# Performance work log

Measured on AMD Instinct MI355X. Metric: run time of the kernel, lower is better.

## Reference

```python
import jax, jax.numpy as jnp
import numpy as np

N_ENT = 30000
ALL_REL = 221
N_DIM = 32
L = 2
EVAL_REL = 86
B = 16
E = 120000


def setup_inputs() -> dict:
    key = jax.random.key(0)
    ks = jax.random.split(key, 16)
    d = N_DIM
    inp = {
        'head': jax.random.randint(ks[0], (B,), 0, N_ENT),
        'tail': jax.random.randint(ks[1], (B,), 0, N_ENT),
        'edge_heads': jax.random.randint(ks[2], (E,), 0, N_ENT),
        'edge_tails': jax.random.randint(ks[3], (E,), 0, N_ENT),
        'edge_rels': jax.random.randint(ks[4], (E,), 0, ALL_REL),
        'edge_weight': jnp.ones((E,), jnp.float32),
        # learned params (xavier-ish scale)
        'ent_emb': jax.random.normal(ks[5], (N_ENT, d), jnp.float32) * 0.05,
        'rel_embs': jax.random.normal(ks[6], (L, ALL_REL, d), jnp.float32) * 0.1,
        'Wlin': jax.random.normal(ks[7], (L, d, d), jnp.float32) * (1.0 / np.sqrt(d)),
        'blin': jnp.zeros((L, d), jnp.float32),
        'Wrel': jax.random.normal(ks[8], (L, 2 * d, 5), jnp.float32) * 0.1,
        'brel': jnp.zeros((L, 5), jnp.float32),
        'Watt': jax.random.normal(ks[9], (L, 5, ALL_REL), jnp.float32) * 0.3,
        'batt': jnp.zeros((L, ALL_REL), jnp.float32),
        'Wr': jax.random.normal(ks[10], (4 * d, EVAL_REL), jnp.float32) * 0.1,
        'br': jnp.zeros((EVAL_REL,), jnp.float32),
    }
    return inp


def _propagate(init_emb, init_idx, ht_embed, rel_embs, Wlin, blin, Wrel, brel,
               Watt, batt, edge_weight, eh, et, er):
    # init_emb: (B, d); hiddens: (n_ent, B, d)
    Bn, d = init_emb.shape
    hid = jnp.zeros((N_ENT, Bn, d), init_emb.dtype)
    hid = hid.at[init_idx, jnp.arange(Bn)].set(init_emb)
    for l in range(L):
        # per-sample relation attention weights: (B, all_rel)
        relw = jax.nn.sigmoid(jax.nn.relu(ht_embed @ Wrel[l] + brel[l]) @ Watt[l] + batt[l])
        # generalized rspmm: out[t] += w * (relw[:, r] * rel_emb[r]) * hid[h]
        msg = hid[eh] * (relw.T[er][:, :, None] * rel_embs[l][er][:, None, :])  # (E, B, d)
        msg = msg * edge_weight[:, None, None]
        hid = jax.ops.segment_sum(msg, et, num_segments=N_ENT)  # (n_ent, B, d)
        hid = jax.nn.relu(hid @ Wlin[l] + blin[l])
    return hid


def reference(head, tail, edge_heads, edge_tails, edge_rels, edge_weight,
              ent_emb, rel_embs, Wlin, blin, Wrel, brel, Watt, batt, Wr, br):
    head_embed = ent_emb[head]  # (B, d)
    tail_embed = ent_emb[tail]
    ht_embed = jnp.concatenate([head_embed, tail_embed], axis=-1)  # (B, 2d)

    # head -> tail propagation
    hid = _propagate(head_embed, head, ht_embed, rel_embs, Wlin, blin, Wrel, brel,
                     Watt, batt, edge_weight, edge_heads, edge_tails, edge_rels)
    tail_hid = hid[tail, jnp.arange(tail.shape[0])]  # (B, d)

    # tail -> head propagation (same KG, same layers, per original code)
    hid = _propagate(tail_embed, tail, ht_embed, rel_embs, Wlin, blin, Wrel, brel,
                     Watt, batt, edge_weight, edge_heads, edge_tails, edge_rels)
    head_hid = hid[head, jnp.arange(head.shape[0])]

    embeddings = jnp.concatenate([head_embed, tail_embed, head_hid, tail_hid], axis=1)
    return embeddings @ Wr + br  # (B, eval_rel)
```

## Files before the change

kernel.cpp:

```cpp
#include <hip/hip_runtime.h>
#include <math.h>

#define N_ENTC 30000
#define ALL_RELC 221
#define NDIM 32
#define EVAL_RELC 86
#define BB 16
#define NE 120000
#define ROW 512
#define NSCAN 120
#define EPB 1000
#define MW 938


__global__ __launch_bounds__(512) void k_scan(
    const int* __restrict__ head, const int* __restrict__ tail,
    const int* __restrict__ eh, const int* __restrict__ et,
    const int* __restrict__ er, const float* __restrict__ ew,
    const float* __restrict__ ent_emb,
    const float* __restrict__ Wrel, const float* __restrict__ brel,
    const float* __restrict__ Watt, const float* __restrict__ batt,
    int4* __restrict__ recs, int* __restrict__ counts,
    float* __restrict__ relwG, float* __restrict__ hidB,
    float* __restrict__ qaccB, unsigned* __restrict__ ticket)
{
    __shared__ unsigned mH[MW], mT[MW];
    __shared__ int s_src[32];
    __shared__ int s_cnt[4];
    __shared__ float s_ht[BB * 64];
    __shared__ float s_h5[BB * 5];
    const int t = threadIdx.x, bid = blockIdx.x;

    if (t < 32) s_src[t] = (t < BB) ? head[t] : tail[t - BB];
    for (int i = t; i < MW; i += 512) { mH[i] = 0u; mT[i] = 0u; }
    if (t < 4) s_cnt[t] = 0;
    __syncthreads();
    if (t < BB) {
        int h = s_src[t], q = s_src[BB + t];
        atomicOr(&mH[h >> 5], 1u << (h & 31));
        atomicOr(&mT[q >> 5], 1u << (q & 31));
    }
    __syncthreads();

    const int e0 = bid * EPB;
    const int4* eh4 = (const int4*)(eh + e0);
    const int4* et4 = (const int4*)(et + e0);
    for (int p = t; p < EPB / 4; p += 512) {
        int4 h4 = eh4[p], t4 = et4[p];
        int hv[4] = {h4.x, h4.y, h4.z, h4.w};
        int tv[4] = {t4.x, t4.y, t4.z, t4.w};
#pragma unroll
        for (int c = 0; c < 4; c++) {
            int e = e0 + 4 * p + c, h = hv[c], tt = tv[c];
            bool hH = (mH[h >> 5] >> (h & 31)) & 1u;
            bool hT = (mT[h >> 5] >> (h & 31)) & 1u;
            bool tT = (mT[tt >> 5] >> (tt & 31)) & 1u;
            bool tH = (mH[tt >> 5] >> (tt & 31)) & 1u;
            if (!(hH | hT | tT | tH)) continue;
            int r = er[e];
            int wb = __float_as_int(ew[e]);
            if (hH) {
                unsigned m = 0;
#pragma unroll
                for (int b = 0; b < BB; b++) m |= (s_src[b] == h) ? (1u << b) : 0u;
                int pos = atomicAdd(&s_cnt[0], 1);
                recs[(size_t)bid * EPB + pos] = make_int4(tt, r | (int)(m << 8), wb, h);
            }
            if (hT) {
                unsigned m = 0;
#pragma unroll
                for (int b = 0; b < BB; b++) m |= (s_src[BB + b] == h) ? (1u << b) : 0u;
                int pos = atomicAdd(&s_cnt[1], 1);
                recs[(size_t)NE + bid * EPB + pos] = make_int4(tt, r | (int)(m << 8), wb, h);
            }
            if (tT) {
                unsigned m = 0;
#pragma unroll
                for (int b = 0; b < BB; b++) m |= (s_src[BB + b] == tt) ? (1u << b) : 0u;
                int canon = __ffs(m) - 1;
                int pos = atomicAdd(&s_cnt[2], 1);
                recs[(size_t)2 * NE + bid * EPB + pos] = make_int4(h, r | (canon << 8), wb, tt);
            }
            if (tH) {
                unsigned m = 0;
#pragma unroll
                for (int b = 0; b < BB; b++) m |= (s_src[b] == tt) ? (1u << b) : 0u;
                int canon = __ffs(m) - 1;
                int pos = atomicAdd(&s_cnt[3], 1);
                recs[(size_t)3 * NE + bid * EPB + pos] = make_int4(h, r | (canon << 8), wb, tt);
            }
        }
    }
    __syncthreads();
    if (t < 4) counts[bid * 4 + t] = s_cnt[t];

    {
        const int wid8 = t >> 6, lane = t & 63;
        float4 z = make_float4(0.f, 0.f, 0.f, 0.f);
        for (int li = 2; li < 4; li++) {
            int c = s_cnt[li];
            float* hb = hidB + (size_t)(li - 2) * N_ENTC * ROW;
            for (int j = wid8; j < c; j += 8) {
                int row = recs[(size_t)li * NE + bid * EPB + j].x;
                float4* p = (float4*)(hb + (size_t)row * ROW);
                p[lane] = z;
                p[lane + 64] = z;
            }
        }
    }

    if (bid == 1) {
        for (int i = t; i < 2 * BB * ROW; i += 512) qaccB[i] = 0.f;
        if (t == 0) *ticket = 0u;
    }
    if (bid == 0) {
        for (int i = t; i < BB * NDIM; i += 512) {
            int b = i >> 5, k = i & 31;
            s_ht[b * 64 + k] = ent_emb[(size_t)s_src[b] * NDIM + k];
            s_ht[b * 64 + 32 + k] = ent_emb[(size_t)s_src[BB + b] * NDIM + k];
        }
        __syncthreads();
        for (int l = 0; l < 2; l++) {
            for (int i = t; i < BB * 5; i += 512) {
                int b = i / 5, j = i % 5;
                float s = brel[l * 5 + j];
                for (int k = 0; k < 64; k++)
                    s += s_ht[b * 64 + k] * Wrel[l * 320 + k * 5 + j];
                s_h5[i] = fmaxf(s, 0.f);
            }
            __syncthreads();
            for (int i = t; i < BB * ALL_RELC; i += 512) {
                int b = i / ALL_RELC, r = i % ALL_RELC;
                float s = batt[l * ALL_RELC + r];
                for (int j = 0; j < 5; j++)
                    s += s_h5[b * 5 + j] * Watt[l * 5 * ALL_RELC + j * ALL_RELC + r];
                relwG[l * BB * ALL_RELC + i] = 1.0f / (1.0f + expf(-s));
            }
            __syncthreads();
        }
    }
}

__global__ __launch_bounds__(256) void k_msg1(
    const int* __restrict__ head, const int* __restrict__ tail,
    const float* __restrict__ ent_emb, const float* __restrict__ rel_embs,
    const int4* __restrict__ recs, const int* __restrict__ counts,
    const float* __restrict__ relwG, float* __restrict__ hidB)
{
    __shared__ int s_src[32];
    const int t = threadIdx.x, bid = blockIdx.x;
    int4 c4 = ((const int4*)counts)[bid];
    if ((c4.x | c4.y) == 0) return;
    if (t < 32) s_src[t] = (t < BB) ? head[t] : tail[t - BB];
    __syncthreads();
    const int wid = t >> 6, lane = t & 63;
    const float4* rv0 = (const float4*)rel_embs;
    for (int d = 0; d < 2; d++) {
        int c = d ? c4.y : c4.x;
        const int4* R = recs + (size_t)d * NE + (size_t)bid * EPB;
        float* hb = hidB + (size_t)d * N_ENTC * ROW;
        for (int j = wid; j < c; j += 4) {
            int4 rec = R[j];
            int tt = rec.x, r = rec.y & 255;
            unsigned msk = ((unsigned)rec.y) >> 8;
            float w = __int_as_float(rec.z);
            float* drow = hb + (size_t)tt * ROW;
#pragma unroll
            for (int ii = 0; ii < 2; ii++) {
                int i4 = lane + 64 * ii, b = i4 >> 3, kq = i4 & 7;
                if (!((msk >> b) & 1u)) continue;
                float cf = relwG[b * ALL_RELC + r] * w;
                float4 sv = ((const float4*)(ent_emb + (size_t)s_src[d * BB + b] * NDIM))[kq];
                float4 rr = rv0[r * 8 + kq];
                atomicAdd(drow + i4 * 4 + 0, sv.x * cf * rr.x);
                atomicAdd(drow + i4 * 4 + 1, sv.y * cf * rr.y);
                atomicAdd(drow + i4 * 4 + 2, sv.z * cf * rr.z);
                atomicAdd(drow + i4 * 4 + 3, sv.w * cf * rr.w);
            }
        }
    }
}

__global__ __launch_bounds__(256) void k_tail2(
    const int* __restrict__ head, const int* __restrict__ tail,
    const float* __restrict__ ent_emb, const float* __restrict__ rel_embs,
    const float* __restrict__ Wlin, const float* __restrict__ blin,
    const float* __restrict__ Wr, const float* __restrict__ br,
    const int4* __restrict__ recs, const int* __restrict__ counts,
    const float* __restrict__ relwG, const float* __restrict__ hidB,
    float* __restrict__ qaccB, unsigned* __restrict__ ticket,
    float* __restrict__ out)
{
    __shared__ float sW[NDIM * NDIM];
    __shared__ float sb[NDIM];
    __shared__ float s_tile[4][512];
    __shared__ int s_src[32];
    __shared__ int s_canon[2][BB];
    __shared__ unsigned s_last;
    const int t = threadIdx.x, bid = blockIdx.x;
    const int wid = t >> 6, lane = t & 63;

    int4 c4 = ((const int4*)counts)[bid];
    if (c4.z | c4.w) {
        for (int i = t; i < NDIM * NDIM; i += 256) sW[i] = Wlin[i];
        if (t < NDIM) sb[t] = blin[t];
        __syncthreads();
        const int b4 = lane >> 2, j0 = (lane & 3) * 8;
        const float* rw1 = relwG + BB * ALL_RELC;
        const float4* rv1 = (const float4*)(rel_embs + (size_t)ALL_RELC * NDIM);
        float* tw = &s_tile[wid][0];
        for (int d = 0; d < 2; d++) {
            int c = d ? c4.w : c4.z;
            const int4* R = recs + (size_t)(2 + d) * NE + (size_t)bid * EPB;
            const float* hb = hidB + (size_t)d * N_ENTC * ROW;
            float* qa = qaccB + (size_t)d * BB * ROW;
            for (int j = wid; j < c; j += 4) {
                int4 rec = R[j];
                int row = rec.x, r = rec.y & 255, canon = (rec.y >> 8) & 15;
                float w = __int_as_float(rec.z);
                const float4* src = (const float4*)(hb + (size_t)row * ROW + b4 * NDIM);
                float h[NDIM];
#pragma unroll
                for (int q = 0; q < 8; q++) {
                    float4 v = src[q];
                    h[q * 4 + 0] = v.x; h[q * 4 + 1] = v.y;
                    h[q * 4 + 2] = v.z; h[q * 4 + 3] = v.w;
                }
                float acc[8];
#pragma unroll
                for (int jj = 0; jj < 8; jj++) acc[jj] = sb[j0 + jj];
#pragma unroll
                for (int k = 0; k < NDIM; k++) {
                    float4 w0 = *(const float4*)&sW[k * NDIM + j0];
                    float4 w1 = *(const float4*)&sW[k * NDIM + j0 + 4];
                    float hk = h[k];
                    acc[0] += hk * w0.x; acc[1] += hk * w0.y;
                    acc[2] += hk * w0.z; acc[3] += hk * w0.w;
                    acc[4] += hk * w1.x; acc[5] += hk * w1.y;
                    acc[6] += hk * w1.z; acc[7] += hk * w1.w;
                }
                float4 o0, o1;
                o0.x = fmaxf(acc[0], 0.f); o0.y = fmaxf(acc[1], 0.f);
                o0.z = fmaxf(acc[2], 0.f); o0.w = fmaxf(acc[3], 0.f);
                o1.x = fmaxf(acc[4], 0.f); o1.y = fmaxf(acc[5], 0.f);
                o1.z = fmaxf(acc[6], 0.f); o1.w = fmaxf(acc[7], 0.f);
                *(float4*)&tw[b4 * NDIM + j0] = o0;
                *(float4*)&tw[b4 * NDIM + j0 + 4] = o1;
                float* drow = qa + canon * ROW;
#pragma unroll
                for (int ii = 0; ii < 2; ii++) {
                    int i4 = lane + 64 * ii, b = i4 >> 3, kq = i4 & 7;
                    float cf = rw1[b * ALL_RELC + r] * w;
                    float4 s = *(const float4*)&tw[b * NDIM + kq * 4];
                    float4 rr = rv1[r * 8 + kq];
                    atomicAdd(drow + i4 * 4 + 0, s.x * cf * rr.x);
                    atomicAdd(drow + i4 * 4 + 1, s.y * cf * rr.y);
                    atomicAdd(drow + i4 * 4 + 2, s.z * cf * rr.z);
                    atomicAdd(drow + i4 * 4 + 3, s.w * cf * rr.w);
                }
            }
        }
    }
    __syncthreads();
    if (t == 0) {
        __builtin_amdgcn_fence(__ATOMIC_RELEASE, "agent");
        s_last = __hip_atomic_fetch_add(ticket, 1u, __ATOMIC_RELAXED,
                                        __HIP_MEMORY_SCOPE_AGENT);
    }
    __syncthreads();
    if (s_last != NSCAN - 1) return;
    if (t == 0) __builtin_amdgcn_fence(__ATOMIC_ACQUIRE, "agent");
    __syncthreads();

    float* sx = &s_tile[0][0];
    for (int i = t; i < NDIM * NDIM; i += 256) sW[i] = Wlin[NDIM * NDIM + i];
    if (t < NDIM) sb[t] = blin[NDIM + t];
    if (t < 32) s_src[t] = (t < BB) ? head[t] : tail[t - BB];
    __syncthreads();
    if (t < 2 * BB) {
        int d = t >> 4, b = t & 15;
        int q = s_src[(1 - d) * BB + b];
        int c = 0;
        for (int bb = 0; bb < BB; bb++)
            if (s_src[(1 - d) * BB + bb] == q) { c = bb; break; }
        s_canon[d][b] = c;
    }
    for (int i = t; i < BB * NDIM; i += 256) {
        int b = i >> 5, k = i & 31;
        sx[b * 128 + k] = ent_emb[(size_t)s_src[b] * NDIM + k];
        sx[b * 128 + 32 + k] = ent_emb[(size_t)s_src[BB + b] * NDIM + k];
    }
    __syncthreads();
    for (int d = 0; d < 2; d++) {
        for (int i = t; i < 512; i += 256) {
            int b = i >> 5, j = i & 31;
            const float* hrow = qaccB + (size_t)d * BB * ROW
                                + s_canon[d][b] * ROW + b * NDIM;
            float s = sb[j];
            for (int k = 0; k < NDIM; k++)
                s += hrow[k] * sW[k * NDIM + j];
            sx[b * 128 + (d == 0 ? 96 : 64) + j] = fmaxf(s, 0.f);
        }
    }
    __syncthreads();
    for (int o = t; o < BB * EVAL_RELC; o += 256) {
        int b = o / EVAL_RELC, r = o % EVAL_RELC;
        float s = br[r];
        for (int k = 0; k < 128; k++)
            s += sx[b * 128 + k] * Wr[k * EVAL_RELC + r];
        out[o] = s;
    }
}

extern "C" void kernel_launch(void* const* d_in, const int* in_sizes, int n_in,
                              void* d_out, int out_size, void* d_ws,
                              size_t ws_size, hipStream_t stream)
{
    const int* head = (const int*)d_in[0];
    const int* tail = (const int*)d_in[1];
    const int* eh = (const int*)d_in[2];
    const int* et = (const int*)d_in[3];
    const int* er = (const int*)d_in[4];
    const float* ew = (const float*)d_in[5];
    const float* ent_emb = (const float*)d_in[6];
    const float* rel_embs = (const float*)d_in[7];
    const float* Wlin = (const float*)d_in[8];
    const float* blin = (const float*)d_in[9];
    const float* Wrel = (const float*)d_in[10];
    const float* brel = (const float*)d_in[11];
    const float* Watt = (const float*)d_in[12];
    const float* batt = (const float*)d_in[13];
    const float* Wr = (const float*)d_in[14];
    const float* br = (const float*)d_in[15];
    float* out = (float*)d_out;
    float* ws = (float*)d_ws;

    float* hidB = ws;
    int4* recs = (int4*)(hidB + (size_t)2 * N_ENTC * ROW);
    int* counts = (int*)(recs + (size_t)4 * NE);
    float* relwG = (float*)(counts + 4 * NSCAN);
    float* qaccB = relwG + 7072;
    unsigned* ticket = (unsigned*)(qaccB + 2 * BB * ROW);

    k_scan<<<NSCAN, 512, 0, stream>>>(head, tail, eh, et, er, ew, ent_emb,
                                      Wrel, brel, Watt, batt,
                                      recs, counts, relwG, hidB, qaccB, ticket);
    k_msg1<<<NSCAN, 256, 0, stream>>>(head, tail, ent_emb, rel_embs,
                                      recs, counts, relwG, hidB);
    k_tail2<<<NSCAN, 256, 0, stream>>>(head, tail, ent_emb, rel_embs,
                                       Wlin, blin, Wr, br, recs, counts,
                                       relwG, hidB, qaccB, ticket, out);
}
```

Measured before the change: 132.0 us.

## Merge message and tail kernels into single-block kernel with edge joins in shared memory

```diff
diff --git a/kernel.cpp b/kernel.cpp
--- a/kernel.cpp
+++ b/kernel.cpp
@@ -7,11 +7,10 @@
 #define EVAL_RELC 86
 #define BB 16
 #define NE 120000
-#define ROW 512
 #define NSCAN 120
 #define EPB 1000
 #define MW 938
-
+#define CAPL 128
 
 __global__ __launch_bounds__(512) void k_scan(
     const int* __restrict__ head, const int* __restrict__ tail,
@@ -21,8 +20,7 @@
     const float* __restrict__ Wrel, const float* __restrict__ brel,
     const float* __restrict__ Watt, const float* __restrict__ batt,
     int4* __restrict__ recs, int* __restrict__ counts,
-    float* __restrict__ relwG, float* __restrict__ hidB,
-    float* __restrict__ qaccB, unsigned* __restrict__ ticket)
+    float* __restrict__ relwG)
 {
     __shared__ unsigned mH[MW], mT[MW];
     __shared__ int s_src[32];
@@ -94,25 +92,6 @@
     __syncthreads();
     if (t < 4) counts[bid * 4 + t] = s_cnt[t];
 
-    {
-        const int wid8 = t >> 6, lane = t & 63;
-        float4 z = make_float4(0.f, 0.f, 0.f, 0.f);
-        for (int li = 2; li < 4; li++) {
-            int c = s_cnt[li];
-            float* hb = hidB + (size_t)(li - 2) * N_ENTC * ROW;
-            for (int j = wid8; j < c; j += 8) {
-                int row = recs[(size_t)li * NE + bid * EPB + j].x;
-                float4* p = (float4*)(hb + (size_t)row * ROW);
-                p[lane] = z;
-                p[lane + 64] = z;
-            }
-        }
-    }
-
-    if (bid == 1) {
-        for (int i = t; i < 2 * BB * ROW; i += 512) qaccB[i] = 0.f;
-        if (t == 0) *ticket = 0u;
-    }
     if (bid == 0) {
         for (int i = t; i < BB * NDIM; i += 512) {
             int b = i >> 5, k = i & 31;
@@ -141,142 +120,37 @@
     }
 }
 
-__global__ __launch_bounds__(256) void k_msg1(
-    const int* __restrict__ head, const int* __restrict__ tail,
-    const float* __restrict__ ent_emb, const float* __restrict__ rel_embs,
-    const int4* __restrict__ recs, const int* __restrict__ counts,
-    const float* __restrict__ relwG, float* __restrict__ hidB)
-{
-    __shared__ int s_src[32];
-    const int t = threadIdx.x, bid = blockIdx.x;
-    int4 c4 = ((const int4*)counts)[bid];
-    if ((c4.x | c4.y) == 0) return;
-    if (t < 32) s_src[t] = (t < BB) ? head[t] : tail[t - BB];
-    __syncthreads();
-    const int wid = t >> 6, lane = t & 63;
-    const float4* rv0 = (const float4*)rel_embs;
-    for (int d = 0; d < 2; d++) {
-        int c = d ? c4.y : c4.x;
-        const int4* R = recs + (size_t)d * NE + (size_t)bid * EPB;
-        float* hb = hidB + (size_t)d * N_ENTC * ROW;
-        for (int j = wid; j < c; j += 4) {
-            int4 rec = R[j];
-            int tt = rec.x, r = rec.y & 255;
-            unsigned msk = ((unsigned)rec.y) >> 8;
-            float w = __int_as_float(rec.z);
-            float* drow = hb + (size_t)tt * ROW;
-#pragma unroll
-            for (int ii = 0; ii < 2; ii++) {
-                int i4 = lane + 64 * ii, b = i4 >> 3, kq = i4 & 7;
-                if (!((msk >> b) & 1u)) continue;
-                float cf = relwG[b * ALL_RELC + r] * w;
-                float4 sv = ((const float4*)(ent_emb + (size_t)s_src[d * BB + b] * NDIM))[kq];
-                float4 rr = rv0[r * 8 + kq];
-                atomicAdd(drow + i4 * 4 + 0, sv.x * cf * rr.x);
-                atomicAdd(drow + i4 * 4 + 1, sv.y * cf * rr.y);
-                atomicAdd(drow + i4 * 4 + 2, sv.z * cf * rr.z);
-                atomicAdd(drow + i4 * 4 + 3, sv.w * cf * rr.w);
-            }
-        }
-    }
-}
-
-__global__ __launch_bounds__(256) void k_tail2(
+__global__ __launch_bounds__(256) void k_all(
     const int* __restrict__ head, const int* __restrict__ tail,
     const float* __restrict__ ent_emb, const float* __restrict__ rel_embs,
     const float* __restrict__ Wlin, const float* __restrict__ blin,
     const float* __restrict__ Wr, const float* __restrict__ br,
     const int4* __restrict__ recs, const int* __restrict__ counts,
-    const float* __restrict__ relwG, const float* __restrict__ hidB,
-    float* __restrict__ qaccB, unsigned* __restrict__ ticket,
+    const float* __restrict__ relwG, int4* __restrict__ gcomp,
     float* __restrict__ out)
 {
+    __shared__ float qacc[BB * 512];
+    __shared__ float tiles[4][512];
+    __shared__ int4 s_l[4][CAPL];
+    __shared__ float s_ht[BB * 64];
     __shared__ float sW[NDIM * NDIM];
-    __shared__ float sb[NDIM];
-    __shared__ float s_tile[4][512];
+    __shared__ float sb_[NDIM];
     __shared__ int s_src[32];
+    __shared__ int s_pref[4][128];
+    __shared__ int s_n[4];
+    __shared__ float s_res[2][512];
     __shared__ int s_canon[2][BB];
-    __shared__ unsigned s_last;
-    const int t = threadIdx.x, bid = blockIdx.x;
+
+    const int t = threadIdx.x;
     const int wid = t >> 6, lane = t & 63;
 
-    int4 c4 = ((const int4*)counts)[bid];
-    if (c4.z | c4.w) {
-        for (int i = t; i < NDIM * NDIM; i += 256) sW[i] = Wlin[i];
-        if (t < NDIM) sb[t] = blin[t];
-        __syncthreads();
-        const int b4 = lane >> 2, j0 = (lane & 3) * 8;
-        const float* rw1 = relwG + BB * ALL_RELC;
-        const float4* rv1 = (const float4*)(rel_embs + (size_t)ALL_RELC * NDIM);
-        float* tw = &s_tile[wid][0];
-        for (int d = 0; d < 2; d++) {
-            int c = d ? c4.w : c4.z;
-            const int4* R = recs + (size_t)(2 + d) * NE + (size_t)bid * EPB;
-            const float* hb = hidB + (size_t)d * N_ENTC * ROW;
-            float* qa = qaccB + (size_t)d * BB * ROW;
-            for (int j = wid; j < c; j += 4) {
-                int4 rec = R[j];
-                int row = rec.x, r = rec.y & 255, canon = (rec.y >> 8) & 15;
-                float w = __int_as_float(rec.z);
-                const float4* src = (const float4*)(hb + (size_t)row * ROW + b4 * NDIM);
-                float h[NDIM];
-#pragma unroll
-                for (int q = 0; q < 8; q++) {
-                    float4 v = src[q];
-                    h[q * 4 + 0] = v.x; h[q * 4 + 1] = v.y;
-                    h[q * 4 + 2] = v.z; h[q * 4 + 3] = v.w;
-                }
-                float acc[8];
-#pragma unroll
-                for (int jj = 0; jj < 8; jj++) acc[jj] = sb[j0 + jj];
-#pragma unroll
-                for (int k = 0; k < NDIM; k++) {
-                    float4 w0 = *(const float4*)&sW[k * NDIM + j0];
-                    float4 w1 = *(const float4*)&sW[k * NDIM + j0 + 4];
-                    float hk = h[k];
-                    acc[0] += hk * w0.x; acc[1] += hk * w0.y;
-                    acc[2] += hk * w0.z; acc[3] += hk * w0.w;
-                    acc[4] += hk * w1.x; acc[5] += hk * w1.y;
-                    acc[6] += hk * w1.z; acc[7] += hk * w1.w;
-                }
-                float4 o0, o1;
-                o0.x = fmaxf(acc[0], 0.f); o0.y = fmaxf(acc[1], 0.f);
-                o0.z = fmaxf(acc[2], 0.f); o0.w = fmaxf(acc[3], 0.f);
-                o1.x = fmaxf(acc[4], 0.f); o1.y = fmaxf(acc[5], 0.f);
-                o1.z = fmaxf(acc[6], 0.f); o1.w = fmaxf(acc[7], 0.f);
-                *(float4*)&tw[b4 * NDIM + j0] = o0;
-                *(float4*)&tw[b4 * NDIM + j0 + 4] = o1;
-                float* drow = qa + canon * ROW;
-#pragma unroll
-                for (int ii = 0; ii < 2; ii++) {
-                    int i4 = lane + 64 * ii, b = i4 >> 3, kq = i4 & 7;
-                    float cf = rw1[b * ALL_RELC + r] * w;
-                    float4 s = *(const float4*)&tw[b * NDIM + kq * 4];
-                    float4 rr = rv1[r * 8 + kq];
-                    atomicAdd(drow + i4 * 4 + 0, s.x * cf * rr.x);
-                    atomicAdd(drow + i4 * 4 + 1, s.y * cf * rr.y);
-                    atomicAdd(drow + i4 * 4 + 2, s.z * cf * rr.z);
-                    atomicAdd(drow + i4 * 4 + 3, s.w * cf * rr.w);
-                }
-            }
-        }
-    }
-    __syncthreads();
-    if (t == 0) {
-        __builtin_amdgcn_fence(__ATOMIC_RELEASE, "agent");
-        s_last = __hip_atomic_fetch_add(ticket, 1u, __ATOMIC_RELAXED,
-                                        __HIP_MEMORY_SCOPE_AGENT);
-    }
-    __syncthreads();
-    if (s_last != NSCAN - 1) return;
-    if (t == 0) __builtin_amdgcn_fence(__ATOMIC_ACQUIRE, "agent");
-    __syncthreads();
-
-    float* sx = &s_tile[0][0];
-    for (int i = t; i < NDIM * NDIM; i += 256) sW[i] = Wlin[NDIM * NDIM + i];
-    if (t < NDIM) sb[t] = blin[NDIM + t];
     if (t < 32) s_src[t] = (t < BB) ? head[t] : tail[t - BB];
     __syncthreads();
+    for (int i = t; i < BB * NDIM; i += 256) {
+        int b = i >> 5, k = i & 31;
+        s_ht[b * 64 + k] = ent_emb[(size_t)s_src[b] * NDIM + k];
+        s_ht[b * 64 + 32 + k] = ent_emb[(size_t)s_src[BB + b] * NDIM + k];
+    }
     if (t < 2 * BB) {
         int d = t >> 4, b = t & 15;
         int q = s_src[(1 - d) * BB + b];
@@ -285,22 +159,133 @@
             if (s_src[(1 - d) * BB + bb] == q) { c = bb; break; }
         s_canon[d][b] = c;
     }
-    for (int i = t; i < BB * NDIM; i += 256) {
-        int b = i >> 5, k = i & 31;
-        sx[b * 128 + k] = ent_emb[(size_t)s_src[b] * NDIM + k];
-        sx[b * 128 + 32 + k] = ent_emb[(size_t)s_src[BB + b] * NDIM + k];
-    }
-    __syncthreads();
+
+    for (int li = 0; li < 4; li++) {
+        for (int i = t; i < 128; i += 256)
+            s_pref[li][i] = (i < NSCAN) ? counts[4 * i + li] : 0;
+        __syncthreads();
+        for (int st = 1; st < 128; st <<= 1) {
+            int v = (t < 128 && t >= st) ? s_pref[li][t - st] : 0;
+            __syncthreads();
+            if (t < 128) s_pref[li][t] += v;
+            __syncthreads();
+        }
+        if (t == 0) s_n[li] = s_pref[li][NSCAN - 1];
+    }
+    for (int li = 0; li < 4; li++) {
+        const int4* src = recs + (size_t)li * NE;
+        int4* gDst = gcomp + (size_t)li * NE;
+        for (int i = t; i < NSCAN; i += 256) {
+            int pe = s_pref[li][i];
+            int c = pe - ((i == 0) ? 0 : s_pref[li][i - 1]);
+            int off = pe - c;
+            for (int k = 0; k < c; k++) {
+                int4 v = src[(size_t)i * EPB + k];
+                int p = off + k;
+                if (p < CAPL) s_l[li][p] = v; else gDst[p - CAPL] = v;
+            }
+        }
+    }
+    __syncthreads();
+
+    const float* rw0 = relwG;
+    const float* rw1 = relwG + BB * ALL_RELC;
+    const float* rel0 = rel_embs;
+    const float* rel1 = rel_embs + (size_t)ALL_RELC * NDIM;
+
     for (int d = 0; d < 2; d++) {
+        for (int i = t; i < BB * 512; i += 256) qacc[i] = 0.f;
+        for (int i = t; i < NDIM * NDIM; i += 256) sW[i] = Wlin[i];
+        if (t < NDIM) sb_[t] = blin[t];
+        __syncthreads();
+
+        const int n1 = s_n[d], n2 = s_n[2 + d];
+        const int4* l1l = s_l[d];
+        const int4* g1 = gcomp + (size_t)d * NE;
+        const int4* l2l = s_l[2 + d];
+        const int4* g2 = gcomp + (size_t)(2 + d) * NE;
+        float* tw = &tiles[wid][0];
+        const int ba = lane >> 3, bbs = ba + 8, kq = lane & 7;
+        const int b4 = lane >> 2, j0 = (lane & 3) * 8;
+
+        for (int j2 = wid; j2 < n2; j2 += 4) {
+            int4 rec2 = (j2 < CAPL) ? l2l[j2] : g2[j2 - CAPL];
+            int hh = rec2.x, r2 = rec2.y & 255, canon = (rec2.y >> 8) & 15;
+            float w2 = __int_as_float(rec2.z);
+            float4 a0 = make_float4(0.f, 0.f, 0.f, 0.f);
+            float4 a1 = make_float4(0.f, 0.f, 0.f, 0.f);
+            for (int j1 = 0; j1 < n1; j1++) {
+                int4 rec1 = (j1 < CAPL) ? l1l[j1] : g1[j1 - CAPL];
+                if (rec1.x != hh) continue;
+                int r1 = rec1.y & 255;
+                unsigned msk = ((unsigned)rec1.y) >> 8;
+                float w1 = __int_as_float(rec1.z);
+                float4 rr = ((const float4*)rel0)[r1 * 8 + kq];
+                if ((msk >> ba) & 1u) {
+                    float cf = rw0[ba * ALL_RELC + r1] * w1;
+                    float4 sv = *(const float4*)&s_ht[ba * 64 + d * 32 + kq * 4];
+                    a0.x += sv.x * cf * rr.x; a0.y += sv.y * cf * rr.y;
+                    a0.z += sv.z * cf * rr.z; a0.w += sv.w * cf * rr.w;
+                }
+                if ((msk >> bbs) & 1u) {
+                    float cf = rw0[bbs * ALL_RELC + r1] * w1;
+                    float4 sv = *(const float4*)&s_ht[bbs * 64 + d * 32 + kq * 4];
+                    a1.x += sv.x * cf * rr.x; a1.y += sv.y * cf * rr.y;
+                    a1.z += sv.z * cf * rr.z; a1.w += sv.w * cf * rr.w;
+                }
+            }
+            *(float4*)&tw[lane * 4] = a0;
+            *(float4*)&tw[(lane + 64) * 4] = a1;
+            const float4* srcT = (const float4*)&tw[b4 * NDIM];
+            float h32[NDIM];
+#pragma unroll
+            for (int q = 0; q < 8; q++) {
+                float4 v = srcT[q];
+                h32[q * 4 + 0] = v.x; h32[q * 4 + 1] = v.y;
+                h32[q * 4 + 2] = v.z; h32[q * 4 + 3] = v.w;
+            }
+            float acc[8];
+#pragma unroll
+            for (int jj = 0; jj < 8; jj++) acc[jj] = sb_[j0 + jj];
+#pragma unroll
+            for (int k = 0; k < NDIM; k++) {
+                float4 w0 = *(const float4*)&sW[k * NDIM + j0];
+                float4 w1v = *(const float4*)&sW[k * NDIM + j0 + 4];
+                float hk = h32[k];
+                acc[0] += hk * w0.x; acc[1] += hk * w0.y;
+                acc[2] += hk * w0.z; acc[3] += hk * w0.w;
+                acc[4] += hk * w1v.x; acc[5] += hk * w1v.y;
+                acc[6] += hk * w1v.z; acc[7] += hk * w1v.w;
+            }
+            float cf2 = rw1[b4 * ALL_RELC + r2] * w2;
+#pragma unroll
+            for (int jj = 0; jj < 8; jj++) {
+                float val = fmaxf(acc[jj], 0.f) * cf2 * rel1[r2 * NDIM + j0 + jj];
+                atomicAdd(&qacc[canon * 512 + b4 * NDIM + j0 + jj], val);
+            }
+        }
+        __syncthreads();
+        for (int i = t; i < NDIM * NDIM; i += 256) sW[i] = Wlin[NDIM * NDIM + i];
+        if (t < NDIM) sb_[t] = blin[NDIM + t];
+        __syncthreads();
         for (int i = t; i < 512; i += 256) {
             int b = i >> 5, j = i & 31;
-            const float* hrow = qaccB + (size_t)d * BB * ROW
-                                + s_canon[d][b] * ROW + b * NDIM;
-            float s = sb[j];
+            const float* hrow = &qacc[s_canon[d][b] * 512 + b * NDIM];
+            float s = sb_[j];
             for (int k = 0; k < NDIM; k++)
                 s += hrow[k] * sW[k * NDIM + j];
-            sx[b * 128 + (d == 0 ? 96 : 64) + j] = fmaxf(s, 0.f);
-        }
+            s_res[d][i] = fmaxf(s, 0.f);
+        }
+        __syncthreads();
+    }
+
+    float* sx = qacc;
+    for (int i = t; i < 512; i += 256) {
+        int b = i >> 5, k = i & 31;
+        sx[b * 128 + k] = s_ht[b * 64 + k];
+        sx[b * 128 + 32 + k] = s_ht[b * 64 + 32 + k];
+        sx[b * 128 + 64 + k] = s_res[1][b * 32 + k];
+        sx[b * 128 + 96 + k] = s_res[0][b * 32 + k];
     }
     __syncthreads();
     for (int o = t; o < BB * EVAL_RELC; o += 256) {
@@ -335,19 +320,14 @@
     float* out = (float*)d_out;
     float* ws = (float*)d_ws;
 
-    float* hidB = ws;
-    int4* recs = (int4*)(hidB + (size_t)2 * N_ENTC * ROW);
-    int* counts = (int*)(recs + (size_t)4 * NE);
+    int4* recs = (int4*)ws;
+    int4* gcomp = recs + (size_t)4 * NE;
+    int* counts = (int*)(gcomp + (size_t)4 * NE);
     float* relwG = (float*)(counts + 4 * NSCAN);
-    float* qaccB = relwG + 7072;
-    unsigned* ticket = (unsigned*)(qaccB + 2 * BB * ROW);
 
     k_scan<<<NSCAN, 512, 0, stream>>>(head, tail, eh, et, er, ew, ent_emb,
                                       Wrel, brel, Watt, batt,
-                                      recs, counts, relwG, hidB, qaccB, ticket);
-    k_msg1<<<NSCAN, 256, 0, stream>>>(head, tail, ent_emb, rel_embs,
-                                      recs, counts, relwG, hidB);
-    k_tail2<<<NSCAN, 256, 0, stream>>>(head, tail, ent_emb, rel_embs,
-                                       Wlin, blin, Wr, br, recs, counts,
-                                       relwG, hidB, qaccB, ticket, out);
+                                      recs, counts, relwG);
+    k_all<<<1, 256, 0, stream>>>(head, tail, ent_emb, rel_embs, Wlin, blin,
+                                 Wr, br, recs, counts, relwG, gcomp, out);
 }
```

New measurement: 359.7 us. 2.73x slower.
